# Kernel tuning notes

Measured on AMD Instinct MI355X. Metric: run time of the kernel, lower is better.

The kernel has to match this reference:

```python
import jax, jax.numpy as jnp
import numpy as np
import math

D_MODEL = 1024
NUM_HEADS = 16
HEAD_DIM = D_MODEL // NUM_HEADS  # 64
THETA = 10000.0
BATCH = 2
SEQ = 2048


def setup_inputs() -> dict:
    key = jax.random.key(0)
    ks = jax.random.split(key, 5)
    scale = 0.02
    return {
        "in_features": jax.random.normal(ks[0], (BATCH, SEQ, D_MODEL), jnp.float32),
        "q_proj": jax.random.normal(ks[1], (D_MODEL, D_MODEL), jnp.float32) * scale,
        "k_proj": jax.random.normal(ks[2], (D_MODEL, D_MODEL), jnp.float32) * scale,
        "v_proj": jax.random.normal(ks[3], (D_MODEL, D_MODEL), jnp.float32) * scale,
        "o_proj": jax.random.normal(ks[4], (D_MODEL, D_MODEL), jnp.float32) * scale,
        "token_positions": jnp.arange(SEQ, dtype=jnp.int32),
    }


def _rope(x, token_positions):
    # x: [b, h, s, head_dim]; interleaved even/odd rotation
    half = HEAD_DIM // 2
    inv_freq = 1.0 / (THETA ** (2.0 * jnp.arange(half, dtype=x.dtype) / HEAD_DIM))
    angle = token_positions.astype(x.dtype)[:, None] * inv_freq[None, :]  # [s, half]
    cos, sin = jnp.cos(angle), jnp.sin(angle)
    x_e, x_o = x[..., ::2], x[..., 1::2]
    r_e = x_e * cos - x_o * sin
    r_o = x_e * sin + x_o * cos
    # interleave back: [..., s, half, 2] -> [..., s, head_dim]
    return jnp.stack([r_e, r_o], axis=-1).reshape(x.shape)


def reference(in_features, q_proj, k_proj, v_proj, o_proj, token_positions):
    b, s, _ = in_features.shape
    # projections: weight layout is [d_out, d_in]
    Q = jnp.einsum('bsd,kd->bsk', in_features, q_proj)
    K = jnp.einsum('bsd,kd->bsk', in_features, k_proj)
    V = jnp.einsum('bsd,kd->bsk', in_features, v_proj)
    # split heads: [b, h, s, head_dim]
    Q = Q.reshape(b, s, NUM_HEADS, HEAD_DIM).transpose(0, 2, 1, 3)
    K = K.reshape(b, s, NUM_HEADS, HEAD_DIM).transpose(0, 2, 1, 3)
    V = V.reshape(b, s, NUM_HEADS, HEAD_DIM).transpose(0, 2, 1, 3)
    Q = _rope(Q, token_positions)
    K = _rope(K, token_positions)
    scores = jnp.einsum('bhnd,bhmd->bhnm', Q, K) / math.sqrt(HEAD_DIM)
    causal = jnp.tril(jnp.ones((s, s), dtype=bool))  # [s, s]
    scores = jnp.where(causal[None, None], scores, -jnp.inf)
    attn = jax.nn.softmax(scores, axis=-1)
    out = jnp.einsum('bhnm,bhmd->bhnd', attn, V)
    out = out.transpose(0, 2, 1, 3).reshape(b, s, D_MODEL)
    return jnp.einsum('bsv,dv->bsd', out, o_proj)
```

## Files before the change

### kernel.cpp

```cpp
#include <hip/hip_runtime.h>
#include <hip/hip_bf16.h>

#define D_MODEL 1024
#define NHEAD   16
#define HDIM    64
#define SEQQ    2048
#define NBATCH  2
#define MROWS   (NBATCH * SEQQ)

typedef unsigned short u16;
typedef __attribute__((ext_vector_type(8))) short short8;
typedef __attribute__((ext_vector_type(4))) float floatx4;

__device__ __forceinline__ u16 f2b(float f) {
    union { __hip_bfloat16 h; u16 u; } cv;
    cv.h = __float2bfloat16(f);
    return cv.u;
}
__device__ __forceinline__ float b2f(u16 u) {
    return __uint_as_float(((unsigned int)u) << 16);
}
__device__ __forceinline__ short8 load8(const u16* p) {
    return *reinterpret_cast<const short8*>(p);
}
__device__ __forceinline__ void async_cp16(const void* g, void* l) {
    __builtin_amdgcn_global_load_lds(
        (const __attribute__((address_space(1))) void*)g,
        (__attribute__((address_space(3))) void*)l, 16, 0, 0);
}

__global__ void cvt_all(const float* __restrict__ X,
                        const float* __restrict__ w0, const float* __restrict__ w1,
                        const float* __restrict__ w2, const float* __restrict__ w3,
                        u16* __restrict__ xo,
                        u16* __restrict__ o0, u16* __restrict__ o1,
                        u16* __restrict__ o2, u16* __restrict__ o3) {
    const int z = blockIdx.y;
    const int n4 = (D_MODEL * D_MODEL) / 4;
    const float* in;
    u16* out;
    if (z < 4) { in = X + (size_t)z * n4 * 4;  out = xo + (size_t)z * n4 * 4; }
    else {
        in  = (z == 4) ? w0 : (z == 5) ? w1 : (z == 6) ? w2 : w3;
        out = (z == 4) ? o0 : (z == 5) ? o1 : (z == 6) ? o2 : o3;
    }
    const int i = blockIdx.x * 256 + threadIdx.x;
    float4 v = reinterpret_cast<const float4*>(in)[i];
    ushort4 o;
    o.x = f2b(v.x); o.y = f2b(v.y); o.z = f2b(v.z); o.w = f2b(v.w);
    reinterpret_cast<ushort4*>(out)[i] = o;
}

__global__ __launch_bounds__(256) void gemm_qkv(
    const u16* __restrict__ A,
    const u16* __restrict__ B0, const u16* __restrict__ B1, const u16* __restrict__ B2,
    u16* __restrict__ C0, u16* __restrict__ C1, u16* __restrict__ C2)
{
    const int K = D_MODEL, N = D_MODEL;
    const u16* Bt = (blockIdx.z == 0) ? B0 : (blockIdx.z == 1 ? B1 : B2);
    u16*       Cp = (blockIdx.z == 0) ? C0 : (blockIdx.z == 1 ? C1 : C2);

    __shared__ __attribute__((aligned(16))) u16 As[128 * 32];
    __shared__ __attribute__((aligned(16))) u16 Bs[128 * 32];

    const int tid  = threadIdx.x;
    const int w    = tid >> 6;
    const int lane = tid & 63;
    const int l15  = lane & 15;
    const int quad = lane >> 4;
    const int wm   = w >> 1, wn = w & 1;
    const int tm   = blockIdx.x * 128, tn = blockIdx.y * 128;

    floatx4 acc[4][4];
#pragma unroll
    for (int i = 0; i < 4; i++)
#pragma unroll
        for (int j = 0; j < 4; j++) {
            floatx4 z = {0.f, 0.f, 0.f, 0.f};
            acc[i][j] = z;
        }

    const int srow = lane >> 2;
    const int scol = (lane & 3) * 8;

    for (int k0 = 0; k0 < K; k0 += 32) {
#pragma unroll
        for (int ch = w; ch < 8; ch += 4) {
            async_cp16(A  + (size_t)(tm + ch * 16 + srow) * K + k0 + scol, &As[ch * 512]);
            async_cp16(Bt + (size_t)(tn + ch * 16 + srow) * K + k0 + scol, &Bs[ch * 512]);
        }
        __syncthreads();

        short8 af[4], bfr[4];
#pragma unroll
        for (int mi = 0; mi < 4; mi++)
            af[mi] = load8(&As[(wm * 64 + mi * 16 + l15) * 32 + quad * 8]);
#pragma unroll
        for (int ni = 0; ni < 4; ni++)
            bfr[ni] = load8(&Bs[(wn * 64 + ni * 16 + l15) * 32 + quad * 8]);
#pragma unroll
        for (int mi = 0; mi < 4; mi++)
#pragma unroll
            for (int ni = 0; ni < 4; ni++)
                acc[mi][ni] = __builtin_amdgcn_mfma_f32_16x16x32_bf16(af[mi], bfr[ni], acc[mi][ni], 0, 0, 0);
        __syncthreads();
    }

#pragma unroll
    for (int mi = 0; mi < 4; mi++)
#pragma unroll
        for (int ni = 0; ni < 4; ni++)
#pragma unroll
            for (int rg = 0; rg < 4; rg++) {
                int row = tm + wm * 64 + mi * 16 + quad * 4 + rg;
                int col = tn + wn * 64 + ni * 16 + l15;
                Cp[(size_t)row * N + col] = f2b(acc[mi][ni][rg]);
            }
}

__global__ void rope_qk(const u16* __restrict__ Qraw, const u16* __restrict__ Kraw,
                        const int* __restrict__ pos, u16* __restrict__ Qt, u16* __restrict__ Kt)
{
    const int gid = blockIdx.x * 256 + threadIdx.x;
    const int j = gid & 31;
    const int s = (gid >> 5) & (SEQQ - 1);
    const int h = (gid >> 16) & (NHEAD - 1);
    const int b = gid >> 20;

    const float p   = (float)pos[s];
    const float inv = expf(-(float)j * (9.210340371976184f / 32.0f));
    float sn, cs;
    sincosf(p * inv, &sn, &cs);

    const size_t ioff = ((size_t)(b * SEQQ + s)) * D_MODEL + h * HDIM + 2 * j;
    const ushort2 qp = *reinterpret_cast<const ushort2*>(&Qraw[ioff]);
    const ushort2 kp = *reinterpret_cast<const ushort2*>(&Kraw[ioff]);
    const float qe = b2f(qp.x), qo = b2f(qp.y);
    const float ke = b2f(kp.x), ko = b2f(kp.y);

    const size_t ooff = (((size_t)(b * NHEAD + h)) * SEQQ + s) * HDIM + 2 * j;
    ushort2 qr;
    qr.x = f2b((qe * cs - qo * sn) * 0.125f);
    qr.y = f2b((qe * sn + qo * cs) * 0.125f);
    ushort2 kr;
    kr.x = f2b(ke * cs - ko * sn);
    kr.y = f2b(ke * sn + ko * cs);
    *reinterpret_cast<ushort2*>(&Qt[ooff]) = qr;
    *reinterpret_cast<ushort2*>(&Kt[ooff]) = kr;
}

__global__ __launch_bounds__(256) void vtrans(const u16* __restrict__ Vraw, u16* __restrict__ Vt)
{
    __shared__ u16 tile[64][65];
    const int s0 = blockIdx.x * 64, h = blockIdx.y, b = blockIdx.z;
    const int t = threadIdx.x;
#pragma unroll
    for (int i = 0; i < 16; i++) {
        int idx = t + i * 256;
        int sl = idx >> 6, dl = idx & 63;
        tile[sl][dl] = Vraw[((size_t)(b * SEQQ + s0 + sl)) * D_MODEL + h * HDIM + dl];
    }
    __syncthreads();
#pragma unroll
    for (int i = 0; i < 16; i++) {
        int idx = t + i * 256;
        int dl = idx >> 6, sl = idx & 63;
        Vt[(((size_t)(b * NHEAD + h)) * HDIM + dl) * SEQQ + s0 + sl] = tile[sl][dl];
    }
}

__global__ __launch_bounds__(512, 2) void attn_kernel(
    const u16* __restrict__ Qt, const u16* __restrict__ Kt, const u16* __restrict__ Vt,
    u16* __restrict__ Out)
{
    const int qblk = (gridDim.x - 1) - blockIdx.x;
    const int h = blockIdx.y, b = blockIdx.z;
    const int tid = threadIdx.x, w = tid >> 6, lane = tid & 63;
    const int l15 = lane & 15, quad = lane >> 4;
    const size_t bh = (size_t)(b * NHEAD + h);
    const u16* Qh = Qt + bh * SEQQ * HDIM;
    const u16* Kh = Kt + bh * SEQQ * HDIM;
    const u16* Vh = Vt + bh * HDIM * SEQQ;
    const int q0w = qblk * 128 + w * 16;
    const int tdiag = q0w >> 6;
    const int tmax  = qblk * 2 + 1;

    __shared__ __attribute__((aligned(16))) u16 Ks[3][64 * 64];
    __shared__ __attribute__((aligned(16))) u16 Vs[3][64 * 64];
    __shared__ __attribute__((aligned(16))) u16 Plds[8][16 * 64];

    short8 qf[2];
#pragma unroll
    for (int kk = 0; kk < 2; kk++)
        qf[kk] = load8(&Qh[(size_t)(q0w + l15) * HDIM + kk * 32 + quad * 8]);

    short8 ones;
#pragma unroll
    for (int i = 0; i < 8; i++) ones[i] = (short)0x3F80;

    floatx4 O[4];
    floatx4 l_acc = {0.f, 0.f, 0.f, 0.f};
#pragma unroll
    for (int c = 0; c < 4; c++) { floatx4 z = {0.f, 0.f, 0.f, 0.f}; O[c] = z; }

    const int rr  = lane >> 3;
    const int swz = ((lane & 7) ^ rr) * 8;
    auto stage = [&](int buf, int tt) {
        const int k0s = tt * 64;
        async_cp16(Kh + (size_t)(k0s + w * 8 + rr) * HDIM + swz, &Ks[buf][w * 512]);
        async_cp16(Vh + (size_t)(w * 8 + rr) * SEQQ + k0s + swz, &Vs[buf][w * 512]);
    };

    const int sw1 = ((quad)     ^ (l15 & 7)) * 8;
    const int sw2 = ((quad + 4) ^ (l15 & 7)) * 8;

    stage(0, 0);
    stage(1, 1);

    for (int t = 0; t <= tmax; ++t) {
        const bool more = (t + 2 <= tmax);
        if (more) asm volatile("s_waitcnt vmcnt(2)" ::: "memory");
        else      asm volatile("s_waitcnt vmcnt(0)" ::: "memory");
        __builtin_amdgcn_s_barrier();
        if (more) stage((t + 2) % 3, t + 2);

        if (t > tdiag) continue;

        const u16* KsB = &Ks[t % 3][0];
        const u16* VsB = &Vs[t % 3][0];
        const int k0 = t * 64;

        floatx4 S[4];
#pragma unroll
        for (int c = 0; c < 4; c++) {
            const int rowb = (c * 16 + l15) * 64;
            floatx4 z = {0.f, 0.f, 0.f, 0.f};
            S[c] = __builtin_amdgcn_mfma_f32_16x16x32_bf16(qf[0], load8(&KsB[rowb + sw1]), z,    0, 0, 0);
            S[c] = __builtin_amdgcn_mfma_f32_16x16x32_bf16(qf[1], load8(&KsB[rowb + sw2]), S[c], 0, 0, 0);
        }

        if (t == tdiag) {
#pragma unroll
            for (int r = 0; r < 4; r++) {
                const int q = q0w + quad * 4 + r;
#pragma unroll
                for (int c = 0; c < 4; c++)
                    if (k0 + c * 16 + l15 > q) S[c][r] = -1e30f;
            }
        }

#pragma unroll
        for (int c = 0; c < 4; c++)
#pragma unroll
            for (int r = 0; r < 4; r++)
                S[c][r] = __expf(S[c][r]);

#pragma unroll
        for (int c = 0; c < 4; c++)
#pragma unroll
            for (int r = 0; r < 4; r++) {
                const int row = quad * 4 + r;
                const int chs = ((c * 2 + (l15 >> 3)) ^ (row & 7)) * 8 + (l15 & 7);
                Plds[w][row * 64 + chs] = f2b(S[c][r]);
            }
        const short8 pf0 = load8(&Plds[w][l15 * 64 + ((quad)     ^ (l15 & 7)) * 8]);
        const short8 pf1 = load8(&Plds[w][l15 * 64 + ((quad + 4) ^ (l15 & 7)) * 8]);

        l_acc = __builtin_amdgcn_mfma_f32_16x16x32_bf16(pf0, ones, l_acc, 0, 0, 0);
        l_acc = __builtin_amdgcn_mfma_f32_16x16x32_bf16(pf1, ones, l_acc, 0, 0, 0);

#pragma unroll
        for (int c2 = 0; c2 < 4; c2++) {
            const int rowb = (c2 * 16 + l15) * 64;
            O[c2] = __builtin_amdgcn_mfma_f32_16x16x32_bf16(pf0, load8(&VsB[rowb + sw1]), O[c2], 0, 0, 0);
            O[c2] = __builtin_amdgcn_mfma_f32_16x16x32_bf16(pf1, load8(&VsB[rowb + sw2]), O[c2], 0, 0, 0);
        }
    }

    float inv_l[4];
#pragma unroll
    for (int r = 0; r < 4; r++) inv_l[r] = 1.0f / l_acc[r];

#pragma unroll
    for (int c2 = 0; c2 < 4; c2++)
#pragma unroll
        for (int r = 0; r < 4; r++) {
            const int q   = q0w + quad * 4 + r;
            const int col = h * HDIM + c2 * 16 + l15;
            Out[(size_t)(b * SEQQ + q) * D_MODEL + col] = f2b(O[c2][r] * inv_l[r]);
        }
}

__global__ __launch_bounds__(256) void gemm_o(
    const u16* __restrict__ A, const u16* __restrict__ Bt, float* __restrict__ C)
{
    const int K = D_MODEL, N = D_MODEL;
    __shared__ __attribute__((aligned(16))) u16 As[64 * 32];
    __shared__ __attribute__((aligned(16))) u16 Bs[128 * 32];

    const int tid  = threadIdx.x;
    const int w    = tid >> 6;
    const int lane = tid & 63;
    const int l15  = lane & 15;
    const int quad = lane >> 4;
    const int wm   = w >> 1, wn = w & 1;
    const int tm   = blockIdx.x * 64, tn = blockIdx.y * 128;

    floatx4 acc[2][4];
#pragma unroll
    for (int i = 0; i < 2; i++)
#pragma unroll
        for (int j = 0; j < 4; j++) {
            floatx4 z = {0.f, 0.f, 0.f, 0.f};
            acc[i][j] = z;
        }

    const int srow = lane >> 2;
    const int scol = (lane & 3) * 8;

    for (int k0 = 0; k0 < K; k0 += 32) {
#pragma unroll
        for (int ch = w; ch < 12; ch += 4) {
            if (ch < 4) async_cp16(A  + (size_t)(tm + ch * 16 + srow) * K + k0 + scol, &As[ch * 512]);
            else        async_cp16(Bt + (size_t)(tn + (ch - 4) * 16 + srow) * K + k0 + scol, &Bs[(ch - 4) * 512]);
        }
        __syncthreads();

        short8 af[2], bfr[4];
#pragma unroll
        for (int mi = 0; mi < 2; mi++)
            af[mi] = load8(&As[(wm * 32 + mi * 16 + l15) * 32 + quad * 8]);
#pragma unroll
        for (int ni = 0; ni < 4; ni++)
            bfr[ni] = load8(&Bs[(wn * 64 + ni * 16 + l15) * 32 + quad * 8]);
#pragma unroll
        for (int mi = 0; mi < 2; mi++)
#pragma unroll
            for (int ni = 0; ni < 4; ni++)
                acc[mi][ni] = __builtin_amdgcn_mfma_f32_16x16x32_bf16(af[mi], bfr[ni], acc[mi][ni], 0, 0, 0);
        __syncthreads();
    }

#pragma unroll
    for (int mi = 0; mi < 2; mi++)
#pragma unroll
        for (int ni = 0; ni < 4; ni++)
#pragma unroll
            for (int rg = 0; rg < 4; rg++) {
                int row = tm + wm * 32 + mi * 16 + quad * 4 + rg;
                int col = tn + wn * 64 + ni * 16 + l15;
                C[(size_t)row * N + col] = acc[mi][ni][rg];
            }
}

extern "C" void kernel_launch(void* const* d_in, const int* in_sizes, int n_in,
                              void* d_out, int out_size, void* d_ws, size_t ws_size,
                              hipStream_t stream)
{
    const float* X  = (const float*)d_in[0];
    const float* Wq = (const float*)d_in[1];
    const float* Wk = (const float*)d_in[2];
    const float* Wv = (const float*)d_in[3];
    const float* Wo = (const float*)d_in[4];
    const int* tpos = (const int*)d_in[5];
    float* out = (float*)d_out;
    char* ws = (char*)d_ws;

    const size_t MB = (size_t)1 << 20;
    u16* Xb   = (u16*)(ws + 0);
    u16* WqB  = (u16*)(ws + 8 * MB);
    u16* WkB  = (u16*)(ws + 10 * MB);
    u16* WvB  = (u16*)(ws + 12 * MB);
    u16* WoB  = (u16*)(ws + 14 * MB);
    u16* Qraw = (u16*)(ws + 16 * MB);
    u16* Kraw = (u16*)(ws + 24 * MB);
    u16* Vraw = (u16*)(ws + 32 * MB);
    u16* Qt   = (u16*)(ws + 40 * MB);
    u16* Kt   = (u16*)(ws + 48 * MB);
    u16* Vt   = Xb;
    u16* AOut = Qraw;

    cvt_all<<<dim3(1024, 8), 256, 0, stream>>>(X, Wq, Wk, Wv, Wo,
                                               Xb, WqB, WkB, WvB, WoB);

    gemm_qkv<<<dim3(32, 8, 3), 256, 0, stream>>>(Xb, WqB, WkB, WvB,
                                                 Qraw, Kraw, Vraw);
    rope_qk<<<8192, 256, 0, stream>>>(Qraw, Kraw, tpos, Qt, Kt);
    vtrans<<<dim3(32, 16, 2), 256, 0, stream>>>(Vraw, Vt);
    attn_kernel<<<dim3(16, 16, 2), 512, 0, stream>>>(Qt, Kt, Vt, AOut);
    gemm_o<<<dim3(64, 8), 256, 0, stream>>>(AOut, WoB, out);
}
```

Baseline: 203.9 us.

## Pair causal query tiles per block and remap block ids across XCDs

The attention kernel now uses 256-thread blocks that each process two 64-row query tiles, one long (31-pr) and one short (pr). This balances causal work so every block does the same number of KV tiles. The flat 512-block grid is remapped so consecutive block ids are spread across heads, probably to fit the XCD round-robin dispatch and L2 locality. Each wave now stages twice as many K/V rows, and the pipeline is restarted between the two phases. That restart adds a drain barrier and a pipeline warmup per phase.

After: 189.0 us. 1.08x faster.

```diff
diff --git a/kernel.cpp b/kernel.cpp
--- a/kernel.cpp
+++ b/kernel.cpp
@@ -169,126 +169,137 @@
     }
 }
 
-__global__ __launch_bounds__(512, 2) void attn_kernel(
+__global__ __launch_bounds__(256, 2) void attn_kernel(
     const u16* __restrict__ Qt, const u16* __restrict__ Kt, const u16* __restrict__ Vt,
     u16* __restrict__ Out)
 {
-    const int qblk = (gridDim.x - 1) - blockIdx.x;
-    const int h = blockIdx.y, b = blockIdx.z;
+    const int bid  = blockIdx.x;
+    const int slot = bid >> 3;
+    const int col  = ((bid & 7) << 2) | (slot >> 4);
+    const int pr   = slot & 15;
+    const int h = col & (NHEAD - 1), b = col >> 4;
+
     const int tid = threadIdx.x, w = tid >> 6, lane = tid & 63;
     const int l15 = lane & 15, quad = lane >> 4;
     const size_t bh = (size_t)(b * NHEAD + h);
     const u16* Qh = Qt + bh * SEQQ * HDIM;
     const u16* Kh = Kt + bh * SEQQ * HDIM;
     const u16* Vh = Vt + bh * HDIM * SEQQ;
-    const int q0w = qblk * 128 + w * 16;
-    const int tdiag = q0w >> 6;
-    const int tmax  = qblk * 2 + 1;
 
     __shared__ __attribute__((aligned(16))) u16 Ks[3][64 * 64];
     __shared__ __attribute__((aligned(16))) u16 Vs[3][64 * 64];
-    __shared__ __attribute__((aligned(16))) u16 Plds[8][16 * 64];
-
-    short8 qf[2];
-#pragma unroll
-    for (int kk = 0; kk < 2; kk++)
-        qf[kk] = load8(&Qh[(size_t)(q0w + l15) * HDIM + kk * 32 + quad * 8]);
+    __shared__ __attribute__((aligned(16))) u16 Plds[4][16 * 64];
 
     short8 ones;
 #pragma unroll
     for (int i = 0; i < 8; i++) ones[i] = (short)0x3F80;
-
-    floatx4 O[4];
-    floatx4 l_acc = {0.f, 0.f, 0.f, 0.f};
-#pragma unroll
-    for (int c = 0; c < 4; c++) { floatx4 z = {0.f, 0.f, 0.f, 0.f}; O[c] = z; }
 
     const int rr  = lane >> 3;
     const int swz = ((lane & 7) ^ rr) * 8;
     auto stage = [&](int buf, int tt) {
         const int k0s = tt * 64;
-        async_cp16(Kh + (size_t)(k0s + w * 8 + rr) * HDIM + swz, &Ks[buf][w * 512]);
-        async_cp16(Vh + (size_t)(w * 8 + rr) * SEQQ + k0s + swz, &Vs[buf][w * 512]);
+        async_cp16(Kh + (size_t)(k0s + w * 8 + rr) * HDIM + swz,       &Ks[buf][w * 512]);
+        async_cp16(Kh + (size_t)(k0s + (w + 4) * 8 + rr) * HDIM + swz, &Ks[buf][(w + 4) * 512]);
+        async_cp16(Vh + (size_t)(w * 8 + rr) * SEQQ + k0s + swz,       &Vs[buf][w * 512]);
+        async_cp16(Vh + (size_t)((w + 4) * 8 + rr) * SEQQ + k0s + swz, &Vs[buf][(w + 4) * 512]);
     };
 
     const int sw1 = ((quad)     ^ (l15 & 7)) * 8;
     const int sw2 = ((quad + 4) ^ (l15 & 7)) * 8;
 
-    stage(0, 0);
-    stage(1, 1);
-
-    for (int t = 0; t <= tmax; ++t) {
-        const bool more = (t + 2 <= tmax);
-        if (more) asm volatile("s_waitcnt vmcnt(2)" ::: "memory");
-        else      asm volatile("s_waitcnt vmcnt(0)" ::: "memory");
-        __builtin_amdgcn_s_barrier();
-        if (more) stage((t + 2) % 3, t + 2);
-
-        if (t > tdiag) continue;
-
-        const u16* KsB = &Ks[t % 3][0];
-        const u16* VsB = &Vs[t % 3][0];
-        const int k0 = t * 64;
-
-        floatx4 S[4];
-#pragma unroll
-        for (int c = 0; c < 4; c++) {
-            const int rowb = (c * 16 + l15) * 64;
-            floatx4 z = {0.f, 0.f, 0.f, 0.f};
-            S[c] = __builtin_amdgcn_mfma_f32_16x16x32_bf16(qf[0], load8(&KsB[rowb + sw1]), z,    0, 0, 0);
-            S[c] = __builtin_amdgcn_mfma_f32_16x16x32_bf16(qf[1], load8(&KsB[rowb + sw2]), S[c], 0, 0, 0);
-        }
-
-        if (t == tdiag) {
+    for (int phase = 0; phase < 2; ++phase) {
+        const int qsub  = phase ? pr : (31 - pr);
+        const int q0w   = qsub * 64 + w * 16;
+        const int tmaxp = qsub;
+
+        if (phase) {
+            asm volatile("s_waitcnt vmcnt(0) lgkmcnt(0)" ::: "memory");
+            __builtin_amdgcn_s_barrier();
+        }
+
+        short8 qf[2];
+#pragma unroll
+        for (int kk = 0; kk < 2; kk++)
+            qf[kk] = load8(&Qh[(size_t)(q0w + l15) * HDIM + kk * 32 + quad * 8]);
+
+        floatx4 O[4];
+        floatx4 l_acc = {0.f, 0.f, 0.f, 0.f};
+#pragma unroll
+        for (int c = 0; c < 4; c++) { floatx4 z = {0.f, 0.f, 0.f, 0.f}; O[c] = z; }
+
+        stage(0, 0);
+        if (tmaxp >= 1) stage(1, 1);
+
+        for (int t = 0; t <= tmaxp; ++t) {
+            if (t < tmaxp) asm volatile("s_waitcnt vmcnt(4)" ::: "memory");
+            else           asm volatile("s_waitcnt vmcnt(0)" ::: "memory");
+            __builtin_amdgcn_s_barrier();
+            if (t + 2 <= tmaxp) stage((t + 2) % 3, t + 2);
+
+            const u16* KsB = &Ks[t % 3][0];
+            const u16* VsB = &Vs[t % 3][0];
+            const int k0 = t * 64;
+
+            floatx4 S[4];
+#pragma unroll
+            for (int c = 0; c < 4; c++) {
+                const int rowb = (c * 16 + l15) * 64;
+                floatx4 z = {0.f, 0.f, 0.f, 0.f};
+                S[c] = __builtin_amdgcn_mfma_f32_16x16x32_bf16(qf[0], load8(&KsB[rowb + sw1]), z,    0, 0, 0);
+                S[c] = __builtin_amdgcn_mfma_f32_16x16x32_bf16(qf[1], load8(&KsB[rowb + sw2]), S[c], 0, 0, 0);
+            }
+
+            if (t == tmaxp) {
+#pragma unroll
+                for (int r = 0; r < 4; r++) {
+                    const int q = q0w + quad * 4 + r;
+#pragma unroll
+                    for (int c = 0; c < 4; c++)
+                        if (k0 + c * 16 + l15 > q) S[c][r] = -1e30f;
+                }
+            }
+
+#pragma unroll
+            for (int c = 0; c < 4; c++)
+#pragma unroll
+                for (int r = 0; r < 4; r++)
+                    S[c][r] = __expf(S[c][r]);
+
+#pragma unroll
+            for (int c = 0; c < 4; c++)
+#pragma unroll
+                for (int r = 0; r < 4; r++) {
+                    const int row = quad * 4 + r;
+                    const int chs = ((c * 2 + (l15 >> 3)) ^ (row & 7)) * 8 + (l15 & 7);
+                    Plds[w][row * 64 + chs] = f2b(S[c][r]);
+                }
+            const short8 pf0 = load8(&Plds[w][l15 * 64 + ((quad)     ^ (l15 & 7)) * 8]);
+            const short8 pf1 = load8(&Plds[w][l15 * 64 + ((quad + 4) ^ (l15 & 7)) * 8]);
+
+            l_acc = __builtin_amdgcn_mfma_f32_16x16x32_bf16(pf0, ones, l_acc, 0, 0, 0);
+            l_acc = __builtin_amdgcn_mfma_f32_16x16x32_bf16(pf1, ones, l_acc, 0, 0, 0);
+
+#pragma unroll
+            for (int c2 = 0; c2 < 4; c2++) {
+                const int rowb = (c2 * 16 + l15) * 64;
+                O[c2] = __builtin_amdgcn_mfma_f32_16x16x32_bf16(pf0, load8(&VsB[rowb + sw1]), O[c2], 0, 0, 0);
+                O[c2] = __builtin_amdgcn_mfma_f32_16x16x32_bf16(pf1, load8(&VsB[rowb + sw2]), O[c2], 0, 0, 0);
+            }
+        }
+
+        float inv_l[4];
+#pragma unroll
+        for (int r = 0; r < 4; r++) inv_l[r] = 1.0f / l_acc[r];
+
+#pragma unroll
+        for (int c2 = 0; c2 < 4; c2++)
 #pragma unroll
             for (int r = 0; r < 4; r++) {
-                const int q = q0w + quad * 4 + r;
-#pragma unroll
-                for (int c = 0; c < 4; c++)
-                    if (k0 + c * 16 + l15 > q) S[c][r] = -1e30f;
-            }
-        }
-
-#pragma unroll
-        for (int c = 0; c < 4; c++)
-#pragma unroll
-            for (int r = 0; r < 4; r++)
-                S[c][r] = __expf(S[c][r]);
-
-#pragma unroll
-        for (int c = 0; c < 4; c++)
-#pragma unroll
-            for (int r = 0; r < 4; r++) {
-                const int row = quad * 4 + r;
-                const int chs = ((c * 2 + (l15 >> 3)) ^ (row & 7)) * 8 + (l15 & 7);
-                Plds[w][row * 64 + chs] = f2b(S[c][r]);
-            }
-        const short8 pf0 = load8(&Plds[w][l15 * 64 + ((quad)     ^ (l15 & 7)) * 8]);
-        const short8 pf1 = load8(&Plds[w][l15 * 64 + ((quad + 4) ^ (l15 & 7)) * 8]);
-
-        l_acc = __builtin_amdgcn_mfma_f32_16x16x32_bf16(pf0, ones, l_acc, 0, 0, 0);
-        l_acc = __builtin_amdgcn_mfma_f32_16x16x32_bf16(pf1, ones, l_acc, 0, 0, 0);
-
-#pragma unroll
-        for (int c2 = 0; c2 < 4; c2++) {
-            const int rowb = (c2 * 16 + l15) * 64;
-            O[c2] = __builtin_amdgcn_mfma_f32_16x16x32_bf16(pf0, load8(&VsB[rowb + sw1]), O[c2], 0, 0, 0);
-            O[c2] = __builtin_amdgcn_mfma_f32_16x16x32_bf16(pf1, load8(&VsB[rowb + sw2]), O[c2], 0, 0, 0);
-        }
-    }
-
-    float inv_l[4];
-#pragma unroll
-    for (int r = 0; r < 4; r++) inv_l[r] = 1.0f / l_acc[r];
-
-#pragma unroll
-    for (int c2 = 0; c2 < 4; c2++)
-#pragma unroll
-        for (int r = 0; r < 4; r++) {
-            const int q   = q0w + quad * 4 + r;
-            const int col = h * HDIM + c2 * 16 + l15;
-            Out[(size_t)(b * SEQQ + q) * D_MODEL + col] = f2b(O[c2][r] * inv_l[r]);
-        }
+                const int q   = q0w + quad * 4 + r;
+                const int colo = h * HDIM + c2 * 16 + l15;
+                Out[(size_t)(b * SEQQ + q) * D_MODEL + colo] = f2b(O[c2][r] * inv_l[r]);
+            }
+    }
 }
 
 __global__ __launch_bounds__(256) void gemm_o(
@@ -387,6 +398,6 @@
                                                  Qraw, Kraw, Vraw);
     rope_qk<<<8192, 256, 0, stream>>>(Qraw, Kraw, tpos, Qt, Kt);
     vtrans<<<dim3(32, 16, 2), 256, 0, stream>>>(Vraw, Vt);
-    attn_kernel<<<dim3(16, 16, 2), 512, 0, stream>>>(Qt, Kt, Vt, AOut);
+    attn_kernel<<<dim3(512, 1, 1), 256, 0, stream>>>(Qt, Kt, Vt, AOut);
     gemm_o<<<dim3(64, 8), 256, 0, stream>>>(AOut, WoB, out);
 }
```
